# Kernel optimization log

Hardware: AMD Instinct MI355X
Metric: run time of the kernel (lower is better)

Reference implementation:

```python
import jax, jax.numpy as jnp
import numpy as np

NUM_HEADS = 16

def _feat(x):
    # tanh feature map mapped to (0,1): (tanh(x)+1)/2
    return (jnp.tanh(x) + 1.0) * 0.5

def setup_inputs() -> dict:
    key = jax.random.key(0)
    k1, k2, k3 = jax.random.split(key, 3)
    B, S, D = 4, 4096, 1024
    q = jax.random.normal(k1, (B, S, D), dtype=jnp.float32)
    k = jax.random.normal(k2, (B, S, D), dtype=jnp.float32)
    v = jax.random.normal(k3, (B, S, D), dtype=jnp.float32)
    return {"q": q, "k": k, "v": v}

def reference(q, k, v):
    B, S, D = q.shape
    H = NUM_HEADS
    d = D // H
    qh = _feat(q.reshape(B, S, H, d))          # (B,S,H,d)
    kh = _feat(k.reshape(B, S, H, d))          # (B,S,H,d)
    vh = v.reshape(B, S, H, d)                 # (B,S,H,e)
    # global kv summary: sum over sequence of outer products k_d v_e per head
    kv = jnp.einsum('bshd,bshe->bdeh', kh, vh)            # (B,d,e,H)
    k_reduced = jnp.sum(kh, axis=1) + 1e-8                # (B,H,d)
    z = 1.0 / jnp.einsum('bshd,bhd->bsh', qh, k_reduced)  # (B,S,H)
    out = jnp.einsum('bshd,bdeh,bsh->bshe', qh, kv, z)    # (B,S,H,e)
    return out.reshape(B, S, H * d)
```

## Files before the change

### kernel.cpp

```cpp
#include <hip/hip_runtime.h>
#include <hip/hip_fp16.h>

#define B_ 4
#define S_ 4096
#define H_ 16
#define D_ 1024
#define HD_ 64
#define NC_ 32

typedef __fp16 hf8 __attribute__((ext_vector_type(8)));
typedef _Float16 h2 __attribute__((ext_vector_type(2)));
typedef float f32x4 __attribute__((ext_vector_type(4)));

__device__ __forceinline__ float featmap(float x) {
  float e = __expf(-2.0f * x);
  return __builtin_amdgcn_rcpf(1.0f + e);
}

__device__ __forceinline__ unsigned pk2u(float a, float b) {
  auto r = __builtin_amdgcn_cvt_pkrtz(a, b);
  unsigned u;
  __builtin_memcpy(&u, &r, 4);
  return u;
}

__device__ __forceinline__ float dot2acc(h2 a, h2 b, float c) {
#if __has_builtin(__builtin_amdgcn_fdot2)
  return __builtin_amdgcn_fdot2(a, b, c, false);
#else
  return c + (float)a[0] * (float)b[0] + (float)a[1] * (float)b[1];
#endif
}

__device__ __forceinline__ int swzf(int d) { return ((d ^ (d >> 2)) & 15) << 4; }

__global__ __launch_bounds__(256, 3) void mh_p1(
    const float* __restrict__ kg, const float* __restrict__ vg,
    __half* __restrict__ kvp, float* __restrict__ kredp) {
  __shared__ __align__(16) char khT[16384];
  __shared__ __align__(16) char vT[16384];
  __shared__ float ksp[256][4];

  const int bid = blockIdx.x;
  const int bh = bid & 63, c = bid >> 6;
  const int b = bh >> 4, h = bh & 15;
  const int t = threadIdx.x, w = t >> 6, l = t & 63;

  const size_t rowbase = (size_t)b * S_ * D_ + (size_t)h * HD_;
  const float* kb = kg + rowbase;
  const float* vb = vg + rowbase;
  const int s0 = c * 128;

  const int cq = (t & 15) * 4;
  const int sgrp = t >> 4;
  float ksacc[4] = {0.f, 0.f, 0.f, 0.f};

  float4 kR[2][4], vR[2][4];
#pragma unroll
  for (int i = 0; i < 2; ++i) {
    const float* kr = kb + (size_t)(s0 + sgrp * 4 + 64 * i) * D_ + cq;
    const float* vr = vb + (size_t)(s0 + sgrp * 4 + 64 * i) * D_ + cq;
#pragma unroll
    for (int r = 0; r < 4; ++r) {
      kR[i][r] = *(const float4*)(kr + r * D_);
      vR[i][r] = *(const float4*)(vr + r * D_);
    }
  }
  __builtin_amdgcn_sched_barrier(0);

#pragma unroll
  for (int i = 0; i < 2; ++i) {
    const int spos = (sgrp * 4 + 64 * i) * 2;
    const float fk[4][4] = {
        {featmap(kR[i][0].x), featmap(kR[i][0].y), featmap(kR[i][0].z), featmap(kR[i][0].w)},
        {featmap(kR[i][1].x), featmap(kR[i][1].y), featmap(kR[i][1].z), featmap(kR[i][1].w)},
        {featmap(kR[i][2].x), featmap(kR[i][2].y), featmap(kR[i][2].z), featmap(kR[i][2].w)},
        {featmap(kR[i][3].x), featmap(kR[i][3].y), featmap(kR[i][3].z), featmap(kR[i][3].w)}};
#pragma unroll
    for (int j = 0; j < 4; ++j) {
      const int d = cq + j;
      const int off = spos ^ swzf(d);
      ksacc[j] += fk[0][j] + fk[1][j] + fk[2][j] + fk[3][j];
      uint2 ku = {pk2u(fk[0][j], fk[1][j]), pk2u(fk[2][j], fk[3][j])};
      uint2 vu = {pk2u(((const float*)&vR[i][0])[j], ((const float*)&vR[i][1])[j]),
                  pk2u(((const float*)&vR[i][2])[j], ((const float*)&vR[i][3])[j])};
      *(uint2*)&khT[d * 256 + off] = ku;
      *(uint2*)&vT [d * 256 + off] = vu;
    }
  }
#pragma unroll
  for (int j = 0; j < 4; ++j) ksp[t][j] = ksacc[j];
  __syncthreads();

  f32x4 acc[4];
#pragma unroll
  for (int et = 0; et < 4; ++et) acc[et] = (f32x4){0.f, 0.f, 0.f, 0.f};
  const int arow = l & 15;
  const int sub = (l >> 4) * 16;
  const int dA = w * 16 + arow;
  const int foA = swzf(dA);
  int foB[4];
#pragma unroll
  for (int et = 0; et < 4; ++et) foB[et] = swzf(et * 16 + arow);

#pragma unroll
  for (int kk = 0; kk < 4; ++kk) {
    const int sbyte = kk * 64 + sub;
    hf8 af;
    {
      float4 tmp = *(const float4*)&khT[dA * 256 + (sbyte ^ foA)];
      __builtin_memcpy(&af, &tmp, 16);
    }
#pragma unroll
    for (int et = 0; et < 4; ++et) {
      hf8 bf;
      float4 tmp = *(const float4*)&vT[(et * 16 + arow) * 256 + (sbyte ^ foB[et])];
      __builtin_memcpy(&bf, &tmp, 16);
      acc[et] = __builtin_amdgcn_mfma_f32_16x16x32_f16(af, bf, acc[et], 0, 0, 0);
    }
  }

  {
    __half* dst = kvp + ((size_t)(c * 64 + bh)) * 4096;
    const int col = l & 15, rg4 = (l >> 4) * 4;
#pragma unroll
    for (int et = 0; et < 4; ++et)
#pragma unroll
      for (int r = 0; r < 4; ++r)
        dst[(w * 16 + rg4 + r) * 64 + et * 16 + col] = __float2half(acc[et][r]);
  }
  if (t < 64) {
    float s = 0.f;
#pragma unroll
    for (int g = 0; g < 16; ++g) s += ksp[(t >> 2) + 16 * g][t & 3];
    kredp[(size_t)(c * 64 + bh) * 64 + t] = s;
  }
}

__global__ __launch_bounds__(256) void mh_p15(
    const __half* __restrict__ kvp, const float* __restrict__ kredp,
    __half* __restrict__ kv, float* __restrict__ kred) {
  const int i = blockIdx.x * 256 + threadIdx.x;
  float s = 0.f;
#pragma unroll
  for (int c = 0; c < NC_; ++c) s += __half2float(kvp[(size_t)c * 262144 + i]);
  kv[i] = __float2half(s);
  if (i < 64 * 64) {
    float r = 0.f;
#pragma unroll
    for (int c = 0; c < NC_; ++c) r += kredp[c * 4096 + i];
    kred[i] = r + 1e-8f;
  }
}

__global__ __launch_bounds__(256, 3) void mh_p2(
    const float* __restrict__ qg, const __half* __restrict__ kvg,
    const float* __restrict__ kredg, float* __restrict__ outg) {
  __shared__ __align__(16) char qt[32768];
  __shared__ __align__(16) char kvT[8192];
  __shared__ __align__(16) char kredh[128];

  const int bid = blockIdx.x;
  const int bh = bid >> 4, chunk = bid & 15;
  const int b = bh >> 4, h = bh & 15;
  const int blockrow = chunk * 256;
  const int t = threadIdx.x, w = t >> 6, l = t & 63;

  const int tr = t >> 4, tc = (t & 15) * 4;
  const int swst = (tr & 7) << 4;
#pragma unroll
  for (int i = 0; i < 16; ++i) {
    const int row = tr + i * 16;
    float4 qv = *(const float4*)&qg[((size_t)(b * S_) + blockrow + row) * D_ + h * HD_ + tc];
    uint2 u = {pk2u(featmap(qv.x), featmap(qv.y)),
               pk2u(featmap(qv.z), featmap(qv.w))};
    *(uint2*)&qt[row * 128 + ((tc * 2) ^ swst)] = u;
  }
#pragma unroll
  for (int i = 0; i < 16; ++i) {
    const int idx = i * 256 + t;
    const int kk = idx >> 6, e = idx & 63;
    *(__half*)&kvT[e * 128 + ((kk * 2) ^ ((e & 7) << 4))] =
        kvg[(size_t)bh * 4096 + idx];
  }
  if (t < 16) {
    float4 kr = *(const float4*)&kredg[bh * 64 + t * 4];
    uint2 u = {pk2u(kr.x, kr.y), pk2u(kr.z, kr.w)};
    *(uint2*)&kredh[t * 8] = u;
  }
  __syncthreads();

  const int col = l & 15;
  const int kB = (l >> 4) * 16;
  const int sw = (l & 7) << 4;

  f32x4 acc[4][4];
#pragma unroll
  for (int i = 0; i < 4; ++i)
#pragma unroll
    for (int j = 0; j < 4; ++j) acc[i][j] = (f32x4){0.f, 0.f, 0.f, 0.f};
  float zf[4];

  h2 kk0[4], kk1[4];
  {
    float4 r0 = *(const float4*)&kredh[kB];
    float4 r1 = *(const float4*)&kredh[64 + kB];
    __builtin_memcpy(kk0, &r0, 16);
    __builtin_memcpy(kk1, &r1, 16);
  }

#pragma unroll
  for (int rt = 0; rt < 4; ++rt) {
    const int row = w * 64 + rt * 16 + col;
    float4 a0r = *(const float4*)&qt[row * 128 + (kB ^ sw)];
    float4 a1r = *(const float4*)&qt[row * 128 + ((64 + kB) ^ sw)];
    hf8 af0, af1;
    __builtin_memcpy(&af0, &a0r, 16);
    __builtin_memcpy(&af1, &a1r, 16);
    h2 aa0[4], aa1[4];
    __builtin_memcpy(aa0, &a0r, 16);
    __builtin_memcpy(aa1, &a1r, 16);
    float zp = 0.f;
#pragma unroll
    for (int j = 0; j < 4; ++j) {
      zp = dot2acc(aa0[j], kk0[j], zp);
      zp = dot2acc(aa1[j], kk1[j], zp);
    }
    zp += __shfl_xor(zp, 16);
    zp += __shfl_xor(zp, 32);
    zf[rt] = __builtin_amdgcn_rcpf(zp);
#pragma unroll
    for (int et = 0; et < 4; ++et) {
      const int er = et * 16 + col;
      float4 b0r = *(const float4*)&kvT[er * 128 + (kB ^ sw)];
      float4 b1r = *(const float4*)&kvT[er * 128 + ((64 + kB) ^ sw)];
      hf8 bf0, bf1;
      __builtin_memcpy(&bf0, &b0r, 16);
      __builtin_memcpy(&bf1, &b1r, 16);
      acc[rt][et] = __builtin_amdgcn_mfma_f32_16x16x32_f16(af0, bf0, acc[rt][et], 0, 0, 0);
      acc[rt][et] = __builtin_amdgcn_mfma_f32_16x16x32_f16(af1, bf1, acc[rt][et], 0, 0, 0);
    }
  }

  const int rg4 = (l >> 4) * 4;
#pragma unroll
  for (int rt = 0; rt < 4; ++rt) {
#pragma unroll
    for (int r = 0; r < 4; ++r) {
      const float zr = __shfl(zf[rt], rg4 + r);
      const int grow = blockrow + w * 64 + rt * 16 + rg4 + r;
      float* op = &outg[((size_t)(b * S_) + grow) * D_ + h * HD_];
#pragma unroll
      for (int et = 0; et < 4; ++et)
        op[et * 16 + col] = acc[rt][et][r] * zr;
    }
  }
}

extern "C" void kernel_launch(void* const* d_in, const int* in_sizes, int n_in,
                              void* d_out, int out_size, void* d_ws, size_t ws_size,
                              hipStream_t stream) {
  const float* q = (const float*)d_in[0];
  const float* k = (const float*)d_in[1];
  const float* v = (const float*)d_in[2];
  float* out = (float*)d_out;
  char* base = (char*)d_ws;

  __half* kv    = (__half*)base;
  float*  kred  = (float*)(base + 524288);
  __half* kvp   = (__half*)(base + 524288 + 16384);
  float*  kredp = (float*)(base + 524288 + 16384 + (size_t)NC_ * 524288);

  mh_p1 <<<64 * NC_, 256, 0, stream>>>(k, v, kvp, kredp);
  mh_p15<<<1024,     256, 0, stream>>>(kvp, kredp, kv, kred);
  mh_p2 <<<64 * 16,  256, 0, stream>>>(q, kv, kred, out);
}
```

Before: 63.83 us.

## Process two heads per block in kv summary kernel with wider row loads

Each block of the key/value summary kernel now covers two adjacent heads over a 128-row chunk, so each half-wave reads a contiguous 512-byte row segment instead of 256 bytes. The number of blocks is halved. LDS staging buffers are doubled, and each wave computes two MFMA row tiles that reuse the same V fragment. Occupancy drops from 3 to 2 blocks per CU, and the LDS stores become narrower 4-byte writes.

```diff
diff --git a/kernel.cpp b/kernel.cpp
--- a/kernel.cpp
+++ b/kernel.cpp
@@ -34,106 +34,108 @@
 
 __device__ __forceinline__ int swzf(int d) { return ((d ^ (d >> 2)) & 15) << 4; }
 
-__global__ __launch_bounds__(256, 3) void mh_p1(
+__global__ __launch_bounds__(256, 2) void mh_p1(
     const float* __restrict__ kg, const float* __restrict__ vg,
     __half* __restrict__ kvp, float* __restrict__ kredp) {
-  __shared__ __align__(16) char khT[16384];
-  __shared__ __align__(16) char vT[16384];
+  __shared__ __align__(16) char khT[2][16384];
+  __shared__ __align__(16) char vT[2][16384];
   __shared__ float ksp[256][4];
 
   const int bid = blockIdx.x;
-  const int bh = bid & 63, c = bid >> 6;
-  const int b = bh >> 4, h = bh & 15;
+  const int hp = bid & 7;
+  const int bc = bid >> 3;
+  const int b = bc >> 5, c = bc & 31;
   const int t = threadIdx.x, w = t >> 6, l = t & 63;
-
-  const size_t rowbase = (size_t)b * S_ * D_ + (size_t)h * HD_;
-  const float* kb = kg + rowbase;
-  const float* vb = vg + rowbase;
   const int s0 = c * 128;
-
-  const int cq = (t & 15) * 4;
-  const int sgrp = t >> 4;
+  const int h0 = hp * 2;
+
+  const float* kb = kg + (size_t)b * S_ * D_ + h0 * HD_;
+  const float* vb = vg + (size_t)b * S_ * D_ + h0 * HD_;
+
+  const int rr = l >> 5;
+  const int dq = l & 31;
+  const int hd = dq >> 4;
+  const int colf = dq * 4;
+
   float ksacc[4] = {0.f, 0.f, 0.f, 0.f};
 
-  float4 kR[2][4], vR[2][4];
-#pragma unroll
-  for (int i = 0; i < 2; ++i) {
-    const float* kr = kb + (size_t)(s0 + sgrp * 4 + 64 * i) * D_ + cq;
-    const float* vr = vb + (size_t)(s0 + sgrp * 4 + 64 * i) * D_ + cq;
-#pragma unroll
-    for (int r = 0; r < 4; ++r) {
-      kR[i][r] = *(const float4*)(kr + r * D_);
-      vR[i][r] = *(const float4*)(vr + r * D_);
-    }
-  }
-  __builtin_amdgcn_sched_barrier(0);
-
-#pragma unroll
-  for (int i = 0; i < 2; ++i) {
-    const int spos = (sgrp * 4 + 64 * i) * 2;
-    const float fk[4][4] = {
-        {featmap(kR[i][0].x), featmap(kR[i][0].y), featmap(kR[i][0].z), featmap(kR[i][0].w)},
-        {featmap(kR[i][1].x), featmap(kR[i][1].y), featmap(kR[i][1].z), featmap(kR[i][1].w)},
-        {featmap(kR[i][2].x), featmap(kR[i][2].y), featmap(kR[i][2].z), featmap(kR[i][2].w)},
-        {featmap(kR[i][3].x), featmap(kR[i][3].y), featmap(kR[i][3].z), featmap(kR[i][3].w)}};
-#pragma unroll
-    for (int j = 0; j < 4; ++j) {
-      const int d = cq + j;
-      const int off = spos ^ swzf(d);
-      ksacc[j] += fk[0][j] + fk[1][j] + fk[2][j] + fk[3][j];
-      uint2 ku = {pk2u(fk[0][j], fk[1][j]), pk2u(fk[2][j], fk[3][j])};
-      uint2 vu = {pk2u(((const float*)&vR[i][0])[j], ((const float*)&vR[i][1])[j]),
-                  pk2u(((const float*)&vR[i][2])[j], ((const float*)&vR[i][3])[j])};
-      *(uint2*)&khT[d * 256 + off] = ku;
-      *(uint2*)&vT [d * 256 + off] = vu;
-    }
-  }
-#pragma unroll
-  for (int j = 0; j < 4; ++j) ksp[t][j] = ksacc[j];
+#pragma unroll
+  for (int j = 0; j < 8; ++j) {
+    const int rA = w * 32 + j * 4 + rr * 2;
+    const float* gk = kb + (size_t)(s0 + rA) * D_ + colf;
+    const float* gv = vb + (size_t)(s0 + rA) * D_ + colf;
+    float4 kqA = *(const float4*)gk;
+    float4 kqB = *(const float4*)(gk + D_);
+    float4 vqA = *(const float4*)gv;
+    float4 vqB = *(const float4*)(gv + D_);
+    const float fA[4] = {featmap(kqA.x), featmap(kqA.y), featmap(kqA.z), featmap(kqA.w)};
+    const float fB[4] = {featmap(kqB.x), featmap(kqB.y), featmap(kqB.z), featmap(kqB.w)};
+    const float vA[4] = {vqA.x, vqA.y, vqA.z, vqA.w};
+    const float vB[4] = {vqB.x, vqB.y, vqB.z, vqB.w};
+    const int pg = w * 16 + j * 2 + rr;
+#pragma unroll
+    for (int jj = 0; jj < 4; ++jj) {
+      const int dh = (dq & 15) * 4 + jj;
+      const int off = (pg * 4) ^ swzf(dh);
+      ksacc[jj] += fA[jj] + fB[jj];
+      *(unsigned*)&khT[hd][dh * 256 + off] = pk2u(fA[jj], fB[jj]);
+      *(unsigned*)&vT [hd][dh * 256 + off] = pk2u(vA[jj], vB[jj]);
+    }
+  }
+#pragma unroll
+  for (int jj = 0; jj < 4; ++jj) ksp[t][jj] = ksacc[jj];
   __syncthreads();
 
-  f32x4 acc[4];
-#pragma unroll
-  for (int et = 0; et < 4; ++et) acc[et] = (f32x4){0.f, 0.f, 0.f, 0.f};
+  const int hh = w & 1;
+  const int dbase = (w >> 1) * 32;
   const int arow = l & 15;
   const int sub = (l >> 4) * 16;
-  const int dA = w * 16 + arow;
-  const int foA = swzf(dA);
-  int foB[4];
-#pragma unroll
-  for (int et = 0; et < 4; ++et) foB[et] = swzf(et * 16 + arow);
+  f32x4 acc[2][4];
+#pragma unroll
+  for (int rt = 0; rt < 2; ++rt)
+#pragma unroll
+    for (int et = 0; et < 4; ++et) acc[rt][et] = (f32x4){0.f, 0.f, 0.f, 0.f};
 
 #pragma unroll
   for (int kk = 0; kk < 4; ++kk) {
     const int sbyte = kk * 64 + sub;
-    hf8 af;
-    {
-      float4 tmp = *(const float4*)&khT[dA * 256 + (sbyte ^ foA)];
-      __builtin_memcpy(&af, &tmp, 16);
+    hf8 af[2];
+#pragma unroll
+    for (int rt = 0; rt < 2; ++rt) {
+      const int dA = dbase + rt * 16 + arow;
+      float4 tmp = *(const float4*)&khT[hh][dA * 256 + (sbyte ^ swzf(dA))];
+      __builtin_memcpy(&af[rt], &tmp, 16);
     }
 #pragma unroll
     for (int et = 0; et < 4; ++et) {
+      const int e = et * 16 + arow;
       hf8 bf;
-      float4 tmp = *(const float4*)&vT[(et * 16 + arow) * 256 + (sbyte ^ foB[et])];
+      float4 tmp = *(const float4*)&vT[hh][e * 256 + (sbyte ^ swzf(e))];
       __builtin_memcpy(&bf, &tmp, 16);
-      acc[et] = __builtin_amdgcn_mfma_f32_16x16x32_f16(af, bf, acc[et], 0, 0, 0);
+      acc[0][et] = __builtin_amdgcn_mfma_f32_16x16x32_f16(af[0], bf, acc[0][et], 0, 0, 0);
+      acc[1][et] = __builtin_amdgcn_mfma_f32_16x16x32_f16(af[1], bf, acc[1][et], 0, 0, 0);
     }
   }
 
   {
-    __half* dst = kvp + ((size_t)(c * 64 + bh)) * 4096;
+    __half* dst = kvp + ((size_t)(c * 64 + b * 16 + h0 + hh)) * 4096;
     const int col = l & 15, rg4 = (l >> 4) * 4;
 #pragma unroll
-    for (int et = 0; et < 4; ++et)
-#pragma unroll
-      for (int r = 0; r < 4; ++r)
-        dst[(w * 16 + rg4 + r) * 64 + et * 16 + col] = __float2half(acc[et][r]);
-  }
-  if (t < 64) {
+    for (int rt = 0; rt < 2; ++rt)
+#pragma unroll
+      for (int et = 0; et < 4; ++et)
+#pragma unroll
+        for (int r = 0; r < 4; ++r)
+          dst[(dbase + rt * 16 + rg4 + r) * 64 + et * 16 + col] =
+              __float2half(acc[rt][et][r]);
+  }
+  if (t < 128) {
     float s = 0.f;
-#pragma unroll
-    for (int g = 0; g < 16; ++g) s += ksp[(t >> 2) + 16 * g][t & 3];
-    kredp[(size_t)(c * 64 + bh) * 64 + t] = s;
+    const int dqr = t >> 2;
+#pragma unroll
+    for (int wv = 0; wv < 4; ++wv)
+      s += ksp[wv * 64 + dqr][t & 3] + ksp[wv * 64 + 32 + dqr][t & 3];
+    kredp[((size_t)(c * 64 + b * 16 + h0 + (t >> 6))) * 64 + (t & 63)] = s;
   }
 }
 
@@ -271,7 +273,7 @@
   __half* kvp   = (__half*)(base + 524288 + 16384);
   float*  kredp = (float*)(base + 524288 + 16384 + (size_t)NC_ * 524288);
 
-  mh_p1 <<<64 * NC_, 256, 0, stream>>>(k, v, kvp, kredp);
-  mh_p15<<<1024,     256, 0, stream>>>(kvp, kredp, kv, kred);
-  mh_p2 <<<64 * 16,  256, 0, stream>>>(q, kv, kred, out);
-}
+  mh_p1 <<<1024,    256, 0, stream>>>(k, v, kvp, kredp);
+  mh_p15<<<1024,    256, 0, stream>>>(kvp, kredp, kv, kred);
+  mh_p2 <<<64 * 16, 256, 0, stream>>>(q, kv, kred, out);
+}
```

Measured after the change: 64.46 us. No clear change (+1.0%).
